# Performance work log

Measured on AMD Instinct MI355X. Metric: run time of the kernel, lower is better.

The kernel has to match this reference:

```python
import jax, jax.numpy as jnp
import numpy as np

MLOG32 = float(np.log(32.0))


def _maxpool(x, k):
    # F.max_pool2d(stride=1, padding=k//2) pads with -inf, matching init value
    pad = k // 2
    return jax.lax.reduce_window(x, -jnp.inf, jax.lax.max, (1, 1, k, k), (1, 1, 1, 1),
                                 ((0, 0), (0, 0), (pad, pad), (pad, pad)))


def _minpool(x, k):
    return -_maxpool(-x, k)


def _local_sum(x, k):
    # conv2d with all-ones kxk kernel, zero padding, same spatial size
    pad = k // 2
    return jax.lax.reduce_window(x, 0.0, jax.lax.add, (1, 1, k, k), (1, 1, 1, 1),
                                 ((0, 0), (0, 0), (pad, pad), (pad, pad)))


def _conv3(x, kern):
    # torch conv2d == cross-correlation == lax conv (no kernel flip)
    return jax.lax.conv_general_dilated(x, kern, (1, 1), ((1, 1), (1, 1)),
                                        dimension_numbers=('NCHW', 'OIHW', 'NCHW'))


def _otsu(gray, bins=32):
    # vectorized per-batch Otsu threshold; gray in [0,1]
    B, _, H, W = gray.shape
    v = gray.reshape(B, -1)
    idx = jnp.clip((v * bins).astype(jnp.int32), 0, bins - 1)  # histc semantics, v==1 -> last bin
    hist = jax.vmap(lambda i: jnp.bincount(i, length=bins))(idx).astype(gray.dtype)
    p = hist / (H * W + 1e-6)
    xs = jnp.linspace(0.0, 1.0, bins, dtype=gray.dtype)
    omega = jnp.cumsum(p, axis=1)
    mu = jnp.cumsum(p * xs[None, :], axis=1)
    mu_t = mu[:, -1:]
    sigma_b2 = (mu_t * omega - mu) ** 2 / (omega * (1.0 - omega) + 1e-8)
    kbest = jnp.argmax(sigma_b2, axis=1)
    edges = jnp.linspace(0.0, 1.0, bins + 1, dtype=gray.dtype)
    return edges[kbest].reshape(B, 1, 1, 1)


def _concept_maps(image_rgb, cell_dilate=10, k_local=9):
    r, g, b = image_rgb[:, 0:1], image_rgb[:, 1:2], image_rgb[:, 2:3]
    gray = jnp.clip(0.5 * (0.299 * r + 0.587 * g + 0.114 * b + 1.0), 0.0, 1.0)
    thr = _otsu(gray)
    nuc = (gray <= thr).astype(gray.dtype)
    # morphological open+close, k=3
    e = _minpool(nuc, 3)
    d = _maxpool(e, 3)
    d = _maxpool(d, 3)
    e2 = _minpool(d, 3)
    nuc = (e2 > 0.5).astype(gray.dtype)
    er = _minpool(nuc, 3)
    boundary = jnp.maximum(nuc - er, 0.0)
    lap_k = jnp.array([[0, 1, 0], [1, -4, 1], [0, 1, 0]], dtype=gray.dtype).reshape(1, 1, 3, 3)
    lap = jnp.abs(_conv3(nuc, lap_k))
    den = _local_sum(boundary, 5) + 1e-6
    roughness = lap * boundary / den
    kx = jnp.array([[1, 0, -1], [2, 0, -2], [1, 0, -1]], dtype=gray.dtype).reshape(1, 1, 3, 3)
    ky = jnp.array([[1, 2, 1], [0, 0, 0], [-1, -2, -1]], dtype=gray.dtype).reshape(1, 1, 3, 3)
    gx = _conv3(gray, kx)
    gy = _conv3(gray, ky)
    ang = jnp.arctan2(gy, gx)
    den_orient = _local_sum(jnp.ones_like(gray), k_local) + 1e-6
    ms = _local_sum(jnp.sin(ang), k_local) / den_orient
    mc = _local_sum(jnp.cos(ang), k_local) / den_orient
    circ_var = 1.0 - jnp.sqrt(ms ** 2 + mc ** 2 + 1e-6)
    kd = cell_dilate if cell_dilate % 2 == 1 else cell_dilate + 1  # force odd
    cell = jnp.minimum(_maxpool(nuc, kd), 1.0)
    A_n = _local_sum(nuc, k_local)
    A_c = jnp.maximum(_local_sum(cell, k_local) - A_n, 1.0)
    nc = A_n / A_c
    g2 = _local_sum(gray * gray, k_local) / den_orient
    g1 = _local_sum(gray, k_local) / den_orient
    ent_like = jnp.log1p(jnp.maximum(g2 - g1 * g1, 0.0))
    z_maps = jnp.concatenate([roughness, circ_var, nc, ent_like], axis=1)
    return z_maps, nuc


def _energy_forward(image_rgb, cal_a, cal_b, alpha_logits, tau_p, Ht, Wt):
    z_maps, nuc = _concept_maps(image_rgb)
    z0 = jnp.log1p(jnp.maximum(z_maps[:, 0:1], 0.0))
    z1 = jnp.clip(z_maps[:, 1:2], 0.0, 1.0)
    z2 = jnp.log1p(jnp.maximum(z_maps[:, 2:3], 0.0))
    z3 = jnp.clip(z_maps[:, 3:4], 0.0, MLOG32)
    z_stable = jnp.concatenate([z0, z1, z2, z3], axis=1)
    z_cal = jax.nn.softplus(cal_a)[None, :, None, None] * z_stable + cal_b[None, :, None, None]
    alpha = jax.nn.softmax(alpha_logits)[None, :, None, None]
    E = jnp.sum(alpha * z_cal, axis=1, keepdims=True)
    B = E.shape[0]
    if (E.shape[2], E.shape[3]) != (Ht, Wt):
        E_t = jax.image.resize(E, (B, 1, Ht, Wt), method='linear')
    else:
        E_t = E
    tau = 0.2 + jax.nn.softplus(tau_p)
    A = jax.nn.softmax((-E_t / tau).reshape(B, 1, Ht * Wt), axis=-1).reshape(B, 1, Ht, Wt)
    return A, z_maps, nuc, E_t


def setup_inputs() -> dict:
    key = jax.random.key(0)
    k1, k2, k3, k4 = jax.random.split(key, 4)
    B, H, W = 16, 512, 512
    image_rgb = 2.0 * jax.random.uniform(k1, (B, 3, H, W), dtype=jnp.float32) - 1.0
    cal_a = 1.0 + 0.1 * jax.random.normal(k2, (4,), jnp.float32)
    cal_b = 0.1 * jax.random.normal(k3, (4,), jnp.float32)
    alpha_logits = 0.1 * jax.random.normal(k4, (4,), jnp.float32)
    tau_p = jnp.float32(0.5)
    return {"image_rgb": image_rgb, "cal_a": cal_a, "cal_b": cal_b,
            "alpha_logits": alpha_logits, "tau_p": tau_p, "target_h": 512, "target_w": 512}


def reference(image_rgb, cal_a, cal_b, alpha_logits, tau_p, target_h, target_w):
    return _energy_forward(image_rgb, cal_a, cal_b, alpha_logits, tau_p, int(target_h), int(target_w))
```

## Files before the change

kernel.cpp:

```cpp
#include <hip/hip_runtime.h>
#include <math.h>
#include <stdint.h>

#define HW 512
#define IMG (HW*HW)
#define GS 49
#define MLOG32f 3.4657359027997265f
#define WFENCE() __asm__ __volatile__("" ::: "memory")

__device__ __forceinline__ float grayf(float r, float g, float b) {
    float t = __fadd_rn(__fadd_rn(__fmul_rn(0.299f, r), __fmul_rn(0.587f, g)), __fmul_rn(0.114f, b));
    float s = __fmul_rn(0.5f, __fadd_rn(t, 1.0f));
    return fminf(fmaxf(s, 0.0f), 1.0f);
}

__device__ __forceinline__ float softplusf(float x) {
    return fmaxf(x, 0.0f) + log1pf(expf(-fabsf(x)));
}

__device__ __forceinline__ float frcp(float x)  { return __builtin_amdgcn_rcpf(x); }
__device__ __forceinline__ float frsq(float x)  { return __builtin_amdgcn_rsqf(x); }
__device__ __forceinline__ float flog1p(float x){ return __logf(1.0f + x); }

__device__ __forceinline__ uint64_t kmask(int lo, int hi) {
    return (1ull << hi) - (1ull << lo);
}

__global__ __launch_bounds__(256) void k_gray_hist(const float* __restrict__ img,
                                                   float* __restrict__ gray,
                                                   int* __restrict__ hist) {
    __shared__ int lh[32];
    int tid = threadIdx.x;
    int b = blockIdx.y;
    if (tid < 32) lh[tid] = 0;
    __syncthreads();
    const float4* rp = (const float4*)(img + (size_t)b * 3 * IMG);
    const float4* gp = (const float4*)(img + (size_t)b * 3 * IMG + IMG);
    const float4* bp = (const float4*)(img + (size_t)b * 3 * IMG + 2 * IMG);
    float4* op = (float4*)(gray + (size_t)b * IMG);
    int i = blockIdx.x * 256 + tid;
    float4 r = rp[i], g = gp[i], bb = bp[i];
    float4 o;
    o.x = grayf(r.x, g.x, bb.x);
    o.y = grayf(r.y, g.y, bb.y);
    o.z = grayf(r.z, g.z, bb.z);
    o.w = grayf(r.w, g.w, bb.w);
    op[i] = o;
    int idx[4];
    idx[0] = min(max((int)(o.x * 32.0f), 0), 31);
    idx[1] = min(max((int)(o.y * 32.0f), 0), 31);
    idx[2] = min(max((int)(o.z * 32.0f), 0), 31);
    idx[3] = min(max((int)(o.w * 32.0f), 0), 31);
    int lane = tid & 63;
    int bin = lane & 31;
    int cnt = 0;
    #pragma unroll
    for (int e = 0; e < 4; e++) {
        int v = idx[e];
        unsigned long long m0 = __ballot((v & 1)  != 0);
        unsigned long long m1 = __ballot((v & 2)  != 0);
        unsigned long long m2 = __ballot((v & 4)  != 0);
        unsigned long long m3 = __ballot((v & 8)  != 0);
        unsigned long long m4 = __ballot((v & 16) != 0);
        unsigned long long mm = (bin & 1)  ? m0 : ~m0;
        mm &= (bin & 2)  ? m1 : ~m1;
        mm &= (bin & 4)  ? m2 : ~m2;
        mm &= (bin & 8)  ? m3 : ~m3;
        mm &= (bin & 16) ? m4 : ~m4;
        cnt += __popcll(mm);
    }
    if (lane < 32) atomicAdd(&lh[bin], cnt);
    __syncthreads();
    if (tid < 32) atomicAdd(&hist[b * 32 + tid], lh[tid]);
}

__global__ void k_otsu_sc(const int* __restrict__ hist,
                          const float* __restrict__ cal_a, const float* __restrict__ cal_b,
                          const float* __restrict__ alpha_logits, const float* __restrict__ tau_p,
                          float* __restrict__ thr, float* __restrict__ sc, int B) {
    int tid = threadIdx.x;
    if (tid < B) {
        const int* h = hist + tid * 32;
        float omega[32], mu[32];
        float co = 0.0f, cm = 0.0f;
        for (int k = 0; k < 32; k++) {
            float pk = (float)h[k] * (1.0f / 262144.0f);
            float xs = (float)((double)k / 31.0);
            co += pk;
            cm += pk * xs;
            omega[k] = co; mu[k] = cm;
        }
        float mu_t = mu[31];
        float best = -1e30f; int kb = 0;
        for (int k = 0; k < 32; k++) {
            float t = mu_t * omega[k] - mu[k];
            float sb = (t * t) / (omega[k] * (1.0f - omega[k]) + 1e-8f);
            if (sb > best) { best = sb; kb = k; }
        }
        thr[tid] = (float)kb * 0.03125f;
    }
    if (tid == 63) {
        float al[4];
        float m = -1e30f;
        for (int c = 0; c < 4; c++) { al[c] = alpha_logits[c]; m = fmaxf(m, al[c]); }
        float e[4]; float s = 0.0f;
        for (int c = 0; c < 4; c++) { e[c] = expf(al[c] - m); s += e[c]; }
        float bias = 0.0f;
        for (int c = 0; c < 4; c++) {
            float alpha = e[c] / s;
            sc[c] = alpha * softplusf(cal_a[c]);
            bias += alpha * cal_b[c];
        }
        sc[4] = bias;
        float tau = 0.2f + softplusf(tau_p[0]);
        sc[5] = tau;
        sc[6] = -1.0f / tau;
    }
}

__global__ __launch_bounds__(256) void k_thresh(const float* __restrict__ gray,
                                                const float* __restrict__ thr,
                                                uint32_t* __restrict__ packed) {
    int b = blockIdx.y;
    int i = blockIdx.x * 256 + threadIdx.x;
    float t = thr[b];
    float v = gray[(size_t)b * IMG + i];
    unsigned long long m = __ballot(v <= t);
    if ((threadIdx.x & 63) == 0)
        *(uint64_t*)&packed[(size_t)b * 8192 + (i >> 5)] = m;
}

__global__ __launch_bounds__(256, 8) void k_maps(const float* __restrict__ gray,
                                              const uint32_t* __restrict__ p0,
                                              float* __restrict__ zmap,
                                              float* __restrict__ nucf,
                                              float* __restrict__ Eout,
                                              const float* __restrict__ sc,
                                              float* __restrict__ expsum) {
    __shared__ __align__(16) char smem[19752];
    float*    gt   = (float*)smem;
    float2*   rsP  = (float2*)(smem + 8232);
    uint64_t* m0   = (uint64_t*)(smem + 8232);
    uint64_t* m1   = m0 + 58;
    uint64_t* dilh = m1 + 58;
    uint64_t* ehr  = dilh + 50;
    uint64_t* nrow = (uint64_t*)(smem + 18728);
    uint64_t* bnd  = nrow + 50;
    uint64_t* cell = bnd + 36;
    int*      rs_nPT = (int*)smem;
    int*      rs_cPT = (int*)(smem + 1408);
    int*      rs_bPT = (int*)(smem + 2816);
    float*    red  = (float*)(smem + 19736);

    int tid = threadIdx.x, b = blockIdx.z;
    int x0 = blockIdx.x * 32, y0 = blockIdx.y * 32;
    int w0 = x0 >> 5;
    const float* gb = gray + (size_t)b * IMG;
    const uint32_t* pb = p0 + (size_t)b * 8192;

    if (tid >= 64) {
        for (int s = tid - 64; s < 504; s += 192) {
            int r = s / 12, c4 = s - r * 12;
            int gy = y0 + r - 5;
            int gxf = (x0 >> 2) + c4 - 2;
            float4 v = make_float4(0.f, 0.f, 0.f, 0.f);
            if ((unsigned)gy < (unsigned)HW && (unsigned)gxf < 128u)
                v = *(const float4*)(gb + gy * HW + (gxf << 2));
            float* dst = &gt[r * GS + (c4 << 2)];
            dst[0] = v.x; dst[1] = v.y; dst[2] = v.z; dst[3] = v.w;
        }
    } else {
        int lane = tid;
        uint64_t mcol = ~0ull;
        if (x0 == 0)   mcol &= ~((1ull << 13) - 1);
        if (x0 == 480) mcol = (1ull << 45) - 1;
        if (lane < 58) {
            int gy = y0 - 13 + lane;
            uint64_t v = 0;
            if ((unsigned)gy < (unsigned)HW) {
                const uint32_t* rowp = pb + gy * 16;
                uint64_t wm = (w0 > 0)  ? rowp[w0 - 1] : 0;
                uint64_t wc = rowp[w0];
                uint64_t wp = (w0 < 15) ? rowp[w0 + 1] : 0;
                v = (wm >> 19) | (wc << 13) | (wp << 45);
            }
            m0[lane] = v;
        }
        WFENCE();
        if (lane >= 1 && lane < 57) {
            uint64_t e = ~0ull;
            #pragma unroll
            for (int dt = -1; dt <= 1; dt++) {
                int q = lane + dt;
                int gy = y0 - 13 + q;
                uint64_t vv = ((unsigned)gy < (unsigned)HW) ? (m0[q] | ~mcol) : ~0ull;
                e &= vv & (vv << 1) & (vv >> 1);
            }
            m1[lane] = e;
        }
        WFENCE();
        if (lane >= 2 && lane < 56) {
            uint64_t d = 0;
            #pragma unroll
            for (int dt = -1; dt <= 1; dt++) {
                int q = lane + dt;
                int gy = y0 - 13 + q;
                uint64_t vv = ((unsigned)gy < (unsigned)HW) ? (m1[q] & mcol) : 0;
                d |= vv | (vv << 1) | (vv >> 1);
            }
            m0[lane] = d;
        }
        WFENCE();
        if (lane >= 3 && lane < 55) {
            uint64_t d = 0;
            #pragma unroll
            for (int dt = -1; dt <= 1; dt++) {
                int q = lane + dt;
                int gy = y0 - 13 + q;
                uint64_t vv = ((unsigned)gy < (unsigned)HW) ? (m0[q] & mcol) : 0;
                d |= vv | (vv << 1) | (vv >> 1);
            }
            m1[lane] = d;
        }
        WFENCE();
        if (lane >= 4 && lane < 54) {
            uint64_t e = ~0ull;
            #pragma unroll
            for (int dt = -1; dt <= 1; dt++) {
                int q = lane + dt;
                int gy = y0 - 13 + q;
                uint64_t vv = ((unsigned)gy < (unsigned)HW) ? (m1[q] | ~mcol) : ~0ull;
                e &= vv & (vv << 1) & (vv >> 1);
            }
            m0[lane] = e;
        }
        WFENCE();
        if (lane < 50) {
            int gy = y0 - 9 + lane;
            uint64_t v = 0;
            if ((unsigned)gy < (unsigned)HW)
                v = ((m0[lane + 4] & mcol) >> 4) & ((1ull << 50) - 1);
            nrow[lane] = v;
        }
        WFENCE();
        uint64_t mwin = kmask(x0 == 0 ? 9 : 0, x0 == 480 ? 41 : 50);
        if (lane < 50) {
            uint64_t v = nrow[lane];
            uint64_t d = v | (v << 1) | (v >> 1);
            d = d | (d << 2) | (d >> 2);
            d = d | (d << 2) | (d >> 2);
            dilh[lane] = d;
        }
        if (lane >= 6 && lane < 44) {
            int y = y0 - 9 + lane;
            uint64_t m = ((unsigned)y < (unsigned)HW) ? mwin : 0;
            uint64_t v = nrow[lane] | ~m;
            ehr[lane] = v & (v << 1) & (v >> 1);
        }
        WFENCE();
        if (lane < 36) {
            int r = lane + 7;
            uint64_t er = ehr[r - 1] & ehr[r] & ehr[r + 1];
            bnd[lane] = nrow[r] & ~er;
        }
        if (lane < 40) {
            int r = lane + 5;
            int y = y0 - 4 + lane;
            uint64_t c = 0;
            #pragma unroll
            for (int d = -5; d <= 5; d++) c |= dilh[r + d];
            uint64_t m = ((unsigned)y < (unsigned)HW) ? mwin : 0;
            cell[lane] = c & m;
        }
    }
    __syncthreads();

    for (int i = tid; i < 320; i += 256) {
        int ly = i >> 3, c0 = (i & 7) << 2;
        int gyb = y0 + ly - 4;
        bool rowok = (unsigned)gyb < (unsigned)HW;
        int gx0 = x0 + c0 - 4;
        int base = ly * GS + c0 + 3;
        float a0p = gt[base],          a1p = gt[base + GS],          a2p = gt[base + 2 * GS];
        float a0q = gt[base + 1],      a1q = gt[base + GS + 1],      a2q = gt[base + 2 * GS + 1];
        float sa[12], ca[12];
        #pragma unroll
        for (int j = 0; j < 12; j++) {
            float a0r = gt[base + 2 + j], a1r = gt[base + GS + 2 + j], a2r = gt[base + 2 * GS + 2 + j];
            float s = 0.0f, c = 0.0f;
            if (rowok && (unsigned)(gx0 + j) < (unsigned)HW) {
                float gxv = (a0p - a0r) + 2.0f * (a1p - a1r) + (a2p - a2r);
                float gyv = (a0p + 2.0f * a0q + a0r) - (a2p + 2.0f * a2q + a2r);
                float r2 = gxv * gxv + gyv * gyv;
                if (r2 > 0.0f) { float ir = frsq(r2); s = gyv * ir; c = gxv * ir; }
                else { s = 0.0f; c = 1.0f; }
            }
            sa[j] = s; ca[j] = c;
            a0p = a0q; a1p = a1q; a2p = a2q;
            a0q = a0r; a1q = a1r; a2q = a2r;
        }
        float ss = sa[0]+sa[1]+sa[2]+sa[3]+sa[4]+sa[5]+sa[6]+sa[7]+sa[8];
        float cs = ca[0]+ca[1]+ca[2]+ca[3]+ca[4]+ca[5]+ca[6]+ca[7]+ca[8];
        #pragma unroll
        for (int q = 0; q < 4; q++) {
            float2 t; t.x = ss; t.y = cs;
            rsP[(c0 + q) * 41 + ly] = t;
            if (q < 3) { ss += sa[9 + q] - sa[q]; cs += ca[9 + q] - ca[q]; }
        }
    }
    __syncthreads();

    int p = tid & 31, py0 = (tid >> 5) << 2;
    int gx = x0 + p;
    float cntx = (float)(min(gx + 4, HW - 1) - max(gx - 4, 0) + 1);
    float z1v[4], z3v[4];
    {
        float2 v[12];
        #pragma unroll
        for (int j = 0; j < 12; j++) v[j] = rsP[p * 41 + py0 + j];
        float ss = v[0].x+v[1].x+v[2].x+v[3].x+v[4].x+v[5].x+v[6].x+v[7].x+v[8].x;
        float cs = v[0].y+v[1].y+v[2].y+v[3].y+v[4].y+v[5].y+v[6].y+v[7].y+v[8].y;
        #pragma unroll
        for (int q = 0; q < 4; q++) {
            int gy = y0 + py0 + q;
            float cnty = (float)(min(gy + 4, HW - 1) - max(gy - 4, 0) + 1);
            float iden = frcp(cnty * cntx + 1e-6f);
            float ms = ss * iden, mc = cs * iden;
            z1v[q] = 1.0f - sqrtf(ms * ms + mc * mc + 1e-6f);
            if (q < 3) { ss += v[9 + q].x - v[q].x; cs += v[9 + q].y - v[q].y; }
        }
    }
    __syncthreads();

    for (int i = tid; i < 320; i += 256) {
        int ly = i >> 3, c0 = (i & 7) << 2;
        const float* gr = &gt[(ly + 1) * GS + c0 + 4];
        float v[12];
        #pragma unroll
        for (int j = 0; j < 12; j++) v[j] = gr[j];
        float gs = v[0]+v[1]+v[2]+v[3]+v[4]+v[5]+v[6]+v[7]+v[8];
        float g2 = v[0]*v[0]+v[1]*v[1]+v[2]*v[2]+v[3]*v[3]+v[4]*v[4]+v[5]*v[5]+v[6]*v[6]+v[7]*v[7]+v[8]*v[8];
        #pragma unroll
        for (int q = 0; q < 4; q++) {
            float2 t; t.x = gs; t.y = g2;
            rsP[(c0 + q) * 41 + ly] = t;
            if (q < 3) {
                gs += v[9 + q] - v[q];
                g2 += v[9 + q] * v[9 + q] - v[q] * v[q];
            }
        }
    }
    __syncthreads();

    {
        float2 v[12];
        #pragma unroll
        for (int j = 0; j < 12; j++) v[j] = rsP[p * 41 + py0 + j];
        float gs = v[0].x+v[1].x+v[2].x+v[3].x+v[4].x+v[5].x+v[6].x+v[7].x+v[8].x;
        float g2 = v[0].y+v[1].y+v[2].y+v[3].y+v[4].y+v[5].y+v[6].y+v[7].y+v[8].y;
        #pragma unroll
        for (int q = 0; q < 4; q++) {
            int gy = y0 + py0 + q;
            float cnty = (float)(min(gy + 4, HW - 1) - max(gy - 4, 0) + 1);
            float iden = frcp(cnty * cntx + 1e-6f);
            float g1 = gs * iden, gq = g2 * iden;
            z3v[q] = flog1p(fmaxf(gq - g1 * g1, 0.0f));
            if (q < 3) { gs += v[9 + q].x - v[q].x; g2 += v[9 + q].y - v[q].y; }
        }
    }
    for (int i = tid; i < 320; i += 256) {
        int rr = i >> 3, p8 = i & 7, pbase = p8 << 2;
        uint64_t rn = nrow[rr + 5], rc = cell[rr];
        int vn = 0, vc = 0;
        #pragma unroll
        for (int e = 0; e < 4; e++) {
            int pp = pbase + e;
            vn |= __popcll((rn >> (pp + 5)) & 0x1FFull) << (e * 8);
            vc |= __popcll((rc >> (pp + 5)) & 0x1FFull) << (e * 8);
        }
        rs_nPT[p8 * 44 + rr] = vn;
        rs_cPT[p8 * 44 + rr] = vc;
    }
    for (int i = tid; i < 288; i += 256) {
        int rr = i >> 3, p8 = i & 7, pbase = p8 << 2;
        uint64_t rb = bnd[rr];
        int vb = 0;
        #pragma unroll
        for (int e = 0; e < 4; e++) {
            int pp = pbase + e;
            vb |= __popcll((rb >> (pp + 7)) & 0x1Full) << (e * 8);
        }
        rs_bPT[p8 * 40 + rr] = vb;
    }
    __syncthreads();

    float w0f = sc[0], w1f = sc[1], w2f = sc[2], w3f = sc[3], bias = sc[4], ntau = sc[6];
    float* z0p = zmap + ((size_t)b * 4 + 0) * IMG;
    float* z1p = zmap + ((size_t)b * 4 + 1) * IMG;
    float* z2p = zmap + ((size_t)b * 4 + 2) * IMG;
    float* z3p = zmap + ((size_t)b * 4 + 3) * IMG;
    float* Ep  = Eout + (size_t)b * IMG;
    float* np  = nucf + (size_t)b * IMG;
    float acc = 0.0f;
    {
        int p8 = p >> 2, sh = (p & 3) << 3;
        int4 na = *(const int4*)&rs_nPT[p8 * 44 + py0];
        int4 nb = *(const int4*)&rs_nPT[p8 * 44 + py0 + 4];
        int4 nc = *(const int4*)&rs_nPT[p8 * 44 + py0 + 8];
        int4 ka = *(const int4*)&rs_cPT[p8 * 44 + py0];
        int4 kb = *(const int4*)&rs_cPT[p8 * 44 + py0 + 4];
        int4 kc = *(const int4*)&rs_cPT[p8 * 44 + py0 + 8];
        int4 ba = *(const int4*)&rs_bPT[p8 * 40 + py0];
        int4 bbv = *(const int4*)&rs_bPT[p8 * 40 + py0 + 4];
        int en[12], ec[12], eb[8];
        en[0]=na.x; en[1]=na.y; en[2]=na.z; en[3]=na.w;
        en[4]=nb.x; en[5]=nb.y; en[6]=nb.z; en[7]=nb.w;
        en[8]=nc.x; en[9]=nc.y; en[10]=nc.z; en[11]=nc.w;
        ec[0]=ka.x; ec[1]=ka.y; ec[2]=ka.z; ec[3]=ka.w;
        ec[4]=kb.x; ec[5]=kb.y; ec[6]=kb.z; ec[7]=kb.w;
        ec[8]=kc.x; ec[9]=kc.y; ec[10]=kc.z; ec[11]=kc.w;
        eb[0]=ba.x; eb[1]=ba.y; eb[2]=ba.z; eb[3]=ba.w;
        eb[4]=bbv.x; eb[5]=bbv.y; eb[6]=bbv.z; eb[7]=bbv.w;
        #pragma unroll
        for (int j = 0; j < 12; j++) { en[j] = (en[j] >> sh) & 0xFF; ec[j] = (ec[j] >> sh) & 0xFF; }
        #pragma unroll
        for (int j = 0; j < 8; j++) eb[j] = (eb[j] >> sh) & 0xFF;
        int An = en[0]+en[1]+en[2]+en[3]+en[4]+en[5]+en[6]+en[7]+en[8];
        int Ac = ec[0]+ec[1]+ec[2]+ec[3]+ec[4]+ec[5]+ec[6]+ec[7]+ec[8];
        int db = eb[0]+eb[1]+eb[2]+eb[3]+eb[4];
        int kk = p + 9;
        #pragma unroll
        for (int q = 0; q < 4; q++) {
            int py = py0 + q;
            int r = py + 9;
            uint64_t rowc = nrow[r];
            int cbit = (int)((rowc >> kk) & 1);
            int nb4  = (int)((nrow[r - 1] >> kk) & 1) + (int)((nrow[r + 1] >> kk) & 1)
                     + (int)((rowc >> (kk - 1)) & 1) + (int)((rowc >> (kk + 1)) & 1);
            int lap = nb4 - 4 * cbit; lap = lap < 0 ? -lap : lap;
            int bc  = (int)((bnd[py + 2] >> kk) & 1);
            float rough = (float)(lap * bc) * frcp((float)db + 1e-6f);
            float z2 = (float)An * frcp(fmaxf((float)(Ac - An), 1.0f));
            float z0s = flog1p(fmaxf(rough, 0.0f));
            float z1s = fminf(fmaxf(z1v[q], 0.0f), 1.0f);
            float z2s = flog1p(fmaxf(z2, 0.0f));
            float z3s = fminf(fmaxf(z3v[q], 0.0f), MLOG32f);
            float E = w0f * z0s + w1f * z1s + w2f * z2s + w3f * z3s + bias;
            int gy = y0 + py;
            size_t o = (size_t)gy * HW + x0 + p;
            z0p[o] = rough;
            z1p[o] = z1v[q];
            z2p[o] = z2;
            z3p[o] = z3v[q];
            Ep[o]  = E;
            np[o]  = (float)cbit;
            acc += __expf(E * ntau);
            if (q < 3) {
                An += en[9 + q] - en[q];
                Ac += ec[9 + q] - ec[q];
                db += eb[5 + q] - eb[q];
            }
        }
    }
    for (int off = 32; off > 0; off >>= 1) acc += __shfl_down(acc, off, 64);
    if ((tid & 63) == 0) red[tid >> 6] = acc;
    __syncthreads();
    if (tid == 0) atomicAdd(&expsum[b], red[0] + red[1] + red[2] + red[3]);
}

__global__ __launch_bounds__(256) void k_softmaxA(const float* __restrict__ E,
                                                  float* __restrict__ A,
                                                  const float* __restrict__ sc,
                                                  const float* __restrict__ expsum) {
    int b = blockIdx.y;
    int i = blockIdx.x * 256 + threadIdx.x;
    float ntau = sc[6];
    float invS = 1.0f / expsum[b];
    const float4* Ep = (const float4*)(E + (size_t)b * IMG);
    float4* Ap = (float4*)(A + (size_t)b * IMG);
    float4 e = Ep[i];
    float4 o;
    o.x = __expf(e.x * ntau) * invS;
    o.y = __expf(e.y * ntau) * invS;
    o.z = __expf(e.z * ntau) * invS;
    o.w = __expf(e.w * ntau) * invS;
    Ap[i] = o;
}

extern "C" void kernel_launch(void* const* d_in, const int* in_sizes, int n_in,
                              void* d_out, int out_size, void* d_ws, size_t ws_size,
                              hipStream_t stream) {
    const float* img   = (const float*)d_in[0];
    const float* cal_a = (const float*)d_in[1];
    const float* cal_b = (const float*)d_in[2];
    const float* alpha = (const float*)d_in[3];
    const float* tau_p = (const float*)d_in[4];
    int B = in_sizes[0] / (3 * IMG);

    float* out  = (float*)d_out;
    float* A    = out;
    float* zmap = out + (size_t)B * IMG;
    float* nuc  = out + (size_t)B * IMG * 5;
    float* E    = out + (size_t)B * IMG * 6;
    float* gray = A;

    int*      hist    = (int*)d_ws;
    float*    expsum  = (float*)d_ws + B * 32;
    float*    thr     = expsum + B;
    float*    sc      = thr + B;
    uint32_t* packed0 = (uint32_t*)d_ws + 1024;

    hipMemsetAsync(d_ws, 0, (size_t)(B * 32 + B) * 4, stream);
    k_gray_hist<<<dim3(IMG / 1024, B), 256, 0, stream>>>(img, gray, hist);
    k_otsu_sc<<<1, 64, 0, stream>>>(hist, cal_a, cal_b, alpha, tau_p, thr, sc, B);
    k_thresh<<<dim3(IMG / 256, B), 256, 0, stream>>>(gray, thr, packed0);
    dim3 tg(HW / 32, HW / 32, B);
    k_maps<<<tg, 256, 0, stream>>>(gray, packed0, zmap, nuc, E, sc, expsum);
    k_softmaxA<<<dim3(IMG / 1024, B), 256, 0, stream>>>(E, A, sc, expsum);
}
```

Measured before the change: 242.9 us.

## Fuse Otsu threshold, binarization and scalar params into the maps kernel

Removes the separate Otsu/scalar kernel and the threshold-packing kernel. Each tile block now computes the Otsu threshold from the histogram itself and builds its 58-row bitmask halo directly from gray with wave ballots. The softmax weights and tau are also recomputed per block. This cuts two launches and the packed-mask round trip through global memory, at the cost of redundant per-block Otsu and scalar work plus extra float reads of the halo from gray.

```diff
diff --git a/kernel.cpp b/kernel.cpp
--- a/kernel.cpp
+++ b/kernel.cpp
@@ -24,6 +24,31 @@
 
 __device__ __forceinline__ uint64_t kmask(int lo, int hi) {
     return (1ull << hi) - (1ull << lo);
+}
+
+__device__ __forceinline__ float otsu_thr(const int* __restrict__ h) {
+    float co = 0.0f, cm = 0.0f;
+    #pragma unroll
+    for (int k = 0; k < 32; k++) {
+        float pk = (float)h[k] * (1.0f / 262144.0f);
+        float xs = (float)((double)k / 31.0);
+        co += pk;
+        cm += pk * xs;
+    }
+    float mu_t = cm;
+    co = 0.0f; cm = 0.0f;
+    float best = -1e30f; int kb = 0;
+    #pragma unroll
+    for (int k = 0; k < 32; k++) {
+        float pk = (float)h[k] * (1.0f / 262144.0f);
+        float xs = (float)((double)k / 31.0);
+        co += pk;
+        cm += pk * xs;
+        float t = mu_t * co - cm;
+        float sb = (t * t) / (co * (1.0f - co) + 1e-8f);
+        if (sb > best) { best = sb; kb = k; }
+    }
+    return (float)kb * 0.03125f;
 }
 
 __global__ __launch_bounds__(256) void k_gray_hist(const float* __restrict__ img,
@@ -74,69 +99,16 @@
     if (tid < 32) atomicAdd(&hist[b * 32 + tid], lh[tid]);
 }
 
-__global__ void k_otsu_sc(const int* __restrict__ hist,
-                          const float* __restrict__ cal_a, const float* __restrict__ cal_b,
-                          const float* __restrict__ alpha_logits, const float* __restrict__ tau_p,
-                          float* __restrict__ thr, float* __restrict__ sc, int B) {
-    int tid = threadIdx.x;
-    if (tid < B) {
-        const int* h = hist + tid * 32;
-        float omega[32], mu[32];
-        float co = 0.0f, cm = 0.0f;
-        for (int k = 0; k < 32; k++) {
-            float pk = (float)h[k] * (1.0f / 262144.0f);
-            float xs = (float)((double)k / 31.0);
-            co += pk;
-            cm += pk * xs;
-            omega[k] = co; mu[k] = cm;
-        }
-        float mu_t = mu[31];
-        float best = -1e30f; int kb = 0;
-        for (int k = 0; k < 32; k++) {
-            float t = mu_t * omega[k] - mu[k];
-            float sb = (t * t) / (omega[k] * (1.0f - omega[k]) + 1e-8f);
-            if (sb > best) { best = sb; kb = k; }
-        }
-        thr[tid] = (float)kb * 0.03125f;
-    }
-    if (tid == 63) {
-        float al[4];
-        float m = -1e30f;
-        for (int c = 0; c < 4; c++) { al[c] = alpha_logits[c]; m = fmaxf(m, al[c]); }
-        float e[4]; float s = 0.0f;
-        for (int c = 0; c < 4; c++) { e[c] = expf(al[c] - m); s += e[c]; }
-        float bias = 0.0f;
-        for (int c = 0; c < 4; c++) {
-            float alpha = e[c] / s;
-            sc[c] = alpha * softplusf(cal_a[c]);
-            bias += alpha * cal_b[c];
-        }
-        sc[4] = bias;
-        float tau = 0.2f + softplusf(tau_p[0]);
-        sc[5] = tau;
-        sc[6] = -1.0f / tau;
-    }
-}
-
-__global__ __launch_bounds__(256) void k_thresh(const float* __restrict__ gray,
-                                                const float* __restrict__ thr,
-                                                uint32_t* __restrict__ packed) {
-    int b = blockIdx.y;
-    int i = blockIdx.x * 256 + threadIdx.x;
-    float t = thr[b];
-    float v = gray[(size_t)b * IMG + i];
-    unsigned long long m = __ballot(v <= t);
-    if ((threadIdx.x & 63) == 0)
-        *(uint64_t*)&packed[(size_t)b * 8192 + (i >> 5)] = m;
-}
-
-__global__ __launch_bounds__(256, 8) void k_maps(const float* __restrict__ gray,
-                                              const uint32_t* __restrict__ p0,
-                                              float* __restrict__ zmap,
-                                              float* __restrict__ nucf,
-                                              float* __restrict__ Eout,
-                                              const float* __restrict__ sc,
-                                              float* __restrict__ expsum) {
+__global__ __launch_bounds__(256, 8) void k_all(const float* __restrict__ gray,
+                                                const int* __restrict__ hist,
+                                                const float* __restrict__ cal_a,
+                                                const float* __restrict__ cal_b,
+                                                const float* __restrict__ alpha_logits,
+                                                const float* __restrict__ tau_p,
+                                                float* __restrict__ zmap,
+                                                float* __restrict__ nucf,
+                                                float* __restrict__ Eout,
+                                                float* __restrict__ expsum) {
     __shared__ __align__(16) char smem[19752];
     float*    gt   = (float*)smem;
     float2*   rsP  = (float2*)(smem + 8232);
@@ -153,10 +125,21 @@
     float*    red  = (float*)(smem + 19736);
 
     int tid = threadIdx.x, b = blockIdx.z;
+    int lane = tid & 63;
     int x0 = blockIdx.x * 32, y0 = blockIdx.y * 32;
-    int w0 = x0 >> 5;
     const float* gb = gray + (size_t)b * IMG;
-    const uint32_t* pb = p0 + (size_t)b * 8192;
+
+    float thrv = otsu_thr(hist + b * 32);
+
+    for (int r = (tid >> 6); r < 58; r += 4) {
+        int gy = y0 - 13 + r;
+        int gx = x0 - 13 + lane;
+        bool ok = ((unsigned)gy < (unsigned)HW) && ((unsigned)gx < (unsigned)HW);
+        float gv = ok ? gb[gy * HW + gx] : 2.0f;
+        uint64_t v = __ballot(ok && (gv <= thrv));
+        if (lane == 0) m0[r] = v;
+    }
+    __syncthreads();
 
     if (tid >= 64) {
         for (int s = tid - 64; s < 504; s += 192) {
@@ -170,107 +153,94 @@
             dst[0] = v.x; dst[1] = v.y; dst[2] = v.z; dst[3] = v.w;
         }
     } else {
-        int lane = tid;
+        int ml = tid;
         uint64_t mcol = ~0ull;
         if (x0 == 0)   mcol &= ~((1ull << 13) - 1);
         if (x0 == 480) mcol = (1ull << 45) - 1;
-        if (lane < 58) {
-            int gy = y0 - 13 + lane;
-            uint64_t v = 0;
-            if ((unsigned)gy < (unsigned)HW) {
-                const uint32_t* rowp = pb + gy * 16;
-                uint64_t wm = (w0 > 0)  ? rowp[w0 - 1] : 0;
-                uint64_t wc = rowp[w0];
-                uint64_t wp = (w0 < 15) ? rowp[w0 + 1] : 0;
-                v = (wm >> 19) | (wc << 13) | (wp << 45);
-            }
-            m0[lane] = v;
-        }
-        WFENCE();
-        if (lane >= 1 && lane < 57) {
+        if (ml >= 1 && ml < 57) {
             uint64_t e = ~0ull;
             #pragma unroll
             for (int dt = -1; dt <= 1; dt++) {
-                int q = lane + dt;
+                int q = ml + dt;
                 int gy = y0 - 13 + q;
                 uint64_t vv = ((unsigned)gy < (unsigned)HW) ? (m0[q] | ~mcol) : ~0ull;
                 e &= vv & (vv << 1) & (vv >> 1);
             }
-            m1[lane] = e;
+            m1[ml] = e;
         }
         WFENCE();
-        if (lane >= 2 && lane < 56) {
+        if (ml >= 2 && ml < 56) {
             uint64_t d = 0;
             #pragma unroll
             for (int dt = -1; dt <= 1; dt++) {
-                int q = lane + dt;
+                int q = ml + dt;
                 int gy = y0 - 13 + q;
                 uint64_t vv = ((unsigned)gy < (unsigned)HW) ? (m1[q] & mcol) : 0;
                 d |= vv | (vv << 1) | (vv >> 1);
             }
-            m0[lane] = d;
+            m0[ml] = d;
         }
         WFENCE();
-        if (lane >= 3 && lane < 55) {
+        if (ml >= 3 && ml < 55) {
             uint64_t d = 0;
             #pragma unroll
             for (int dt = -1; dt <= 1; dt++) {
-                int q = lane + dt;
+                int q = ml + dt;
                 int gy = y0 - 13 + q;
                 uint64_t vv = ((unsigned)gy < (unsigned)HW) ? (m0[q] & mcol) : 0;
                 d |= vv | (vv << 1) | (vv >> 1);
             }
-            m1[lane] = d;
+            m1[ml] = d;
         }
         WFENCE();
-        if (lane >= 4 && lane < 54) {
+        if (ml >= 4 && ml < 54) {
             uint64_t e = ~0ull;
             #pragma unroll
             for (int dt = -1; dt <= 1; dt++) {
-                int q = lane + dt;
+                int q = ml + dt;
                 int gy = y0 - 13 + q;
                 uint64_t vv = ((unsigned)gy < (unsigned)HW) ? (m1[q] | ~mcol) : ~0ull;
                 e &= vv & (vv << 1) & (vv >> 1);
             }
-            m0[lane] = e;
+            m0[ml] = e;
         }
         WFENCE();
-        if (lane < 50) {
-            int gy = y0 - 9 + lane;
+        if (ml < 50) {
+            int gy = y0 - 9 + ml;
             uint64_t v = 0;
             if ((unsigned)gy < (unsigned)HW)
-                v = ((m0[lane + 4] & mcol) >> 4) & ((1ull << 50) - 1);
-            nrow[lane] = v;
+                v = ((m0[ml + 4] & mcol) >> 4) & ((1ull << 50) - 1);
+            nrow[ml] = v;
         }
         WFENCE();
         uint64_t mwin = kmask(x0 == 0 ? 9 : 0, x0 == 480 ? 41 : 50);
-        if (lane < 50) {
-            uint64_t v = nrow[lane];
+        if (ml < 50) {
+            uint64_t v = nrow[ml];
             uint64_t d = v | (v << 1) | (v >> 1);
             d = d | (d << 2) | (d >> 2);
             d = d | (d << 2) | (d >> 2);
-            dilh[lane] = d;
-        }
-        if (lane >= 6 && lane < 44) {
-            int y = y0 - 9 + lane;
+            dilh[ml] = d;
+        }
+        if (ml >= 6 && ml < 44) {
+            int y = y0 - 9 + ml;
             uint64_t m = ((unsigned)y < (unsigned)HW) ? mwin : 0;
-            uint64_t v = nrow[lane] | ~m;
-            ehr[lane] = v & (v << 1) & (v >> 1);
+            uint64_t v = nrow[ml] | ~m;
+            ehr[ml] = v & (v << 1) & (v >> 1);
         }
         WFENCE();
-        if (lane < 36) {
-            int r = lane + 7;
+        if (ml < 36) {
+            int r = ml + 7;
             uint64_t er = ehr[r - 1] & ehr[r] & ehr[r + 1];
-            bnd[lane] = nrow[r] & ~er;
-        }
-        if (lane < 40) {
-            int r = lane + 5;
-            int y = y0 - 4 + lane;
+            bnd[ml] = nrow[r] & ~er;
+        }
+        if (ml < 40) {
+            int r = ml + 5;
+            int y = y0 - 4 + ml;
             uint64_t c = 0;
             #pragma unroll
             for (int d = -5; d <= 5; d++) c |= dilh[r + d];
             uint64_t m = ((unsigned)y < (unsigned)HW) ? mwin : 0;
-            cell[lane] = c & m;
+            cell[ml] = c & m;
         }
     }
     __syncthreads();
@@ -394,7 +364,23 @@
     }
     __syncthreads();
 
-    float w0f = sc[0], w1f = sc[1], w2f = sc[2], w3f = sc[3], bias = sc[4], ntau = sc[6];
+    float w0f, w1f, w2f, w3f, bias, ntau;
+    {
+        float al[4];
+        float m = -1e30f;
+        for (int c = 0; c < 4; c++) { al[c] = alpha_logits[c]; m = fmaxf(m, al[c]); }
+        float e[4]; float s = 0.0f;
+        for (int c = 0; c < 4; c++) { e[c] = expf(al[c] - m); s += e[c]; }
+        float wv[4]; float bi = 0.0f;
+        for (int c = 0; c < 4; c++) {
+            float alpha = e[c] / s;
+            wv[c] = alpha * softplusf(cal_a[c]);
+            bi += alpha * cal_b[c];
+        }
+        w0f = wv[0]; w1f = wv[1]; w2f = wv[2]; w3f = wv[3]; bias = bi;
+        float tau = 0.2f + softplusf(tau_p[0]);
+        ntau = -1.0f / tau;
+    }
     float* z0p = zmap + ((size_t)b * 4 + 0) * IMG;
     float* z1p = zmap + ((size_t)b * 4 + 1) * IMG;
     float* z2p = zmap + ((size_t)b * 4 + 2) * IMG;
@@ -470,11 +456,12 @@
 
 __global__ __launch_bounds__(256) void k_softmaxA(const float* __restrict__ E,
                                                   float* __restrict__ A,
-                                                  const float* __restrict__ sc,
+                                                  const float* __restrict__ tau_p,
                                                   const float* __restrict__ expsum) {
     int b = blockIdx.y;
     int i = blockIdx.x * 256 + threadIdx.x;
-    float ntau = sc[6];
+    float tau = 0.2f + softplusf(tau_p[0]);
+    float ntau = -1.0f / tau;
     float invS = 1.0f / expsum[b];
     const float4* Ep = (const float4*)(E + (size_t)b * IMG);
     float4* Ap = (float4*)(A + (size_t)b * IMG);
@@ -506,15 +493,10 @@
 
     int*      hist    = (int*)d_ws;
     float*    expsum  = (float*)d_ws + B * 32;
-    float*    thr     = expsum + B;
-    float*    sc      = thr + B;
-    uint32_t* packed0 = (uint32_t*)d_ws + 1024;
 
     hipMemsetAsync(d_ws, 0, (size_t)(B * 32 + B) * 4, stream);
     k_gray_hist<<<dim3(IMG / 1024, B), 256, 0, stream>>>(img, gray, hist);
-    k_otsu_sc<<<1, 64, 0, stream>>>(hist, cal_a, cal_b, alpha, tau_p, thr, sc, B);
-    k_thresh<<<dim3(IMG / 256, B), 256, 0, stream>>>(gray, thr, packed0);
     dim3 tg(HW / 32, HW / 32, B);
-    k_maps<<<tg, 256, 0, stream>>>(gray, packed0, zmap, nuc, E, sc, expsum);
-    k_softmaxA<<<dim3(IMG / 1024, B), 256, 0, stream>>>(E, A, sc, expsum);
-}
+    k_all<<<tg, 256, 0, stream>>>(gray, hist, cal_a, cal_b, alpha, tau_p, zmap, nuc, E, expsum);
+    k_softmaxA<<<dim3(IMG / 1024, B), 256, 0, stream>>>(E, A, tau_p, expsum);
+}
```

Measured after the change: 255.8 us. +5.3%, slower.
